# Kernel optimization log

Hardware: AMD Instinct MI355X
Metric: run time of the kernel (lower is better)

The kernel has to match this reference:

```python
import jax, jax.numpy as jnp
import numpy as np

B, C, H, W, D = 2, 96, 64, 64, 32
NUM_HEADS = 8

def setup_inputs() -> dict:
    key = jax.random.key(0)
    kx, kq, kk, kv, kp = jax.random.split(key, 5)
    x = jax.random.normal(kx, (B, C, H, W, D), dtype=jnp.float32)
    # torch nn.Linear weights: [out_features, in_features]; 1x1x1 conv proj as [C_out, C_in]
    s = 0.02
    Wq = jax.random.normal(kq, (C, C), dtype=jnp.float32) * s
    Wk = jax.random.normal(kk, (C, C), dtype=jnp.float32) * s
    Wv = jax.random.normal(kv, (C, C), dtype=jnp.float32) * s
    Wproj = jax.random.normal(kp, (C, C), dtype=jnp.float32) * s
    return {"x": x, "Wq": Wq, "Wk": Wk, "Wv": Wv, "Wproj": Wproj}

def reference(x, Wq, Wk, Wv, Wproj):
    b, c, h, w, d = x.shape
    n = h * w * d
    nh = NUM_HEADS
    hd = c // nh  # head dim (qk_dim == v_dim == dim here)
    # [B, C, H, W, D] -> [B, N, C]
    xf = jnp.transpose(x.reshape(b, c, n), (0, 2, 1))
    def to_heads(W):
        y = jnp.einsum('bnc,oc->bno', xf, W)  # nn.Linear: x @ W^T
        return jnp.transpose(y.reshape(b, n, nh, hd), (0, 2, 1, 3))  # [B, H, N, hd]
    q = to_heads(Wq)
    k = to_heads(Wk)
    v = to_heads(Wv)
    q = jax.nn.softmax(q, axis=-1)   # over head dim
    k = jax.nn.softmax(k, axis=-2)   # over tokens N
    # linear attention: contract over N first -> tiny [B, H, hd, hd] context
    context = jnp.einsum('bhnd,bhne->bhde', k, v)
    attn = jnp.einsum('bhnd,bhde->bhne', q, context)  # [B, H, N, hd]
    out = jnp.transpose(attn, (0, 2, 1, 3)).reshape(b, n, c)  # [B, N, C]
    out = jnp.transpose(out, (0, 2, 1)).reshape(b, c, h, w, d)
    # 1x1x1 conv projection (bias=False) == channel mixing
    out = jnp.einsum('oc,bchwd->bohwd', Wproj, out)
    return out
```

## Files before the change

kernel.cpp:

```cpp
#include <hip/hip_runtime.h>


typedef _Float16 half_t;
typedef _Float16 half8 __attribute__((ext_vector_type(8)));
typedef float f32x4 __attribute__((ext_vector_type(4)));

#define MFMA16 __builtin_amdgcn_mfma_f32_16x16x32_f16
#define NSH 17
#define NP 16

__global__ __launch_bounds__(256, 2)
void p1(const float* __restrict__ x, const float* __restrict__ Wk,
        const float* __restrict__ Wv, float* __restrict__ part) {
  __shared__ __align__(16) char smem[73792];
  half_t* xs  = (half_t*)smem;
  half_t* wsm = (half_t*)(smem + 26624);
  half_t* vl  = (half_t*)smem;
  half_t* ke  = (half_t*)(smem + 46592);

  const int tid  = threadIdx.x;
  const int lane = tid & 63, l15 = lane & 15, quad = lane >> 4, wid = tid >> 6;
  const int b  = blockIdx.x >> 10;
  const int n0 = (blockIdx.x & 1023) << 7;

  {
    const int n = tid & 127, cg = tid >> 7;
    const float* xb = x + (((size_t)(b * 96 + cg * 48)) << NSH) + n0 + n;
#pragma unroll
    for (int i = 0; i < 48; ++i)
      xs[n * 104 + cg * 48 + i] = (half_t)xb[(size_t)i << NSH];
  }
#pragma unroll
  for (int i = 0; i < 36; ++i) {
    int id = i * 256 + tid; int o = id / 96, c = id - o * 96;
    wsm[o * 104 + c] = (half_t)Wk[id];
  }
  __syncthreads();

  f32x4 acc[6][2];
#pragma unroll
  for (int rt = 0; rt < 6; ++rt)
#pragma unroll
    for (int ct = 0; ct < 2; ++ct) acc[rt][ct] = (f32x4){0.f, 0.f, 0.f, 0.f};
#pragma unroll
  for (int ks = 0; ks < 3; ++ks) {
    half8 af[6], bf[2];
#pragma unroll
    for (int rt = 0; rt < 6; ++rt)
      af[rt] = *(const half8*)&wsm[(rt * 16 + l15) * 104 + ks * 32 + quad * 8];
#pragma unroll
    for (int ct = 0; ct < 2; ++ct)
      bf[ct] = *(const half8*)&xs[((wid * 2 + ct) * 16 + l15) * 104 + ks * 32 + quad * 8];
#pragma unroll
    for (int rt = 0; rt < 6; ++rt)
#pragma unroll
      for (int ct = 0; ct < 2; ++ct)
        acc[rt][ct] = MFMA16(af[rt], bf[ct], acc[rt][ct], 0, 0, 0);
  }
#pragma unroll
  for (int rt = 0; rt < 6; ++rt)
#pragma unroll
    for (int ct = 0; ct < 2; ++ct)
#pragma unroll
      for (int i = 0; i < 4; ++i) {
        int row = rt * 16 + quad * 4 + i;
        int col = (wid * 2 + ct) * 16 + l15;
        ke[row * 136 + col] = (half_t)__expf(acc[rt][ct][i]);
      }
  __syncthreads();

#pragma unroll
  for (int i = 0; i < 36; ++i) {
    int id = i * 256 + tid; int o = id / 96, c = id - o * 96;
    wsm[o * 104 + c] = (half_t)Wv[id];
  }
  __syncthreads();

#pragma unroll
  for (int rt = 0; rt < 6; ++rt)
#pragma unroll
    for (int ct = 0; ct < 2; ++ct) acc[rt][ct] = (f32x4){0.f, 0.f, 0.f, 0.f};
#pragma unroll
  for (int ks = 0; ks < 3; ++ks) {
    half8 af[6], bf[2];
#pragma unroll
    for (int rt = 0; rt < 6; ++rt)
      af[rt] = *(const half8*)&wsm[(rt * 16 + l15) * 104 + ks * 32 + quad * 8];
#pragma unroll
    for (int ct = 0; ct < 2; ++ct)
      bf[ct] = *(const half8*)&xs[((wid * 2 + ct) * 16 + l15) * 104 + ks * 32 + quad * 8];
#pragma unroll
    for (int rt = 0; rt < 6; ++rt)
#pragma unroll
      for (int ct = 0; ct < 2; ++ct)
        acc[rt][ct] = MFMA16(af[rt], bf[ct], acc[rt][ct], 0, 0, 0);
  }
  __syncthreads();
#pragma unroll
  for (int rt = 0; rt < 6; ++rt)
#pragma unroll
    for (int ct = 0; ct < 2; ++ct)
#pragma unroll
      for (int i = 0; i < 4; ++i) {
        int row = rt * 16 + quad * 4 + i;
        int col = (wid * 2 + ct) * 16 + l15;
        vl[row * 136 + col] = (half_t)acc[rt][ct][i];
      }
  __syncthreads();

  float* dst = part + (size_t)((blockIdx.x & (NP - 1)) * 2 + b) * 1248;
#pragma unroll
  for (int hh = 0; hh < 2; ++hh) {
    const int h = wid * 2 + hh;
    f32x4 c = (f32x4){0.f, 0.f, 0.f, 0.f};
#pragma unroll
    for (int ks = 0; ks < 4; ++ks) {
      half8 a  = *(const half8*)&ke[(h * 12 + l15) * 136 + ks * 32 + quad * 8];
      half8 bv = *(const half8*)&vl[(h * 12 + l15) * 136 + ks * 32 + quad * 8];
      c = MFMA16(a, bv, c, 0, 0, 0);
    }
#pragma unroll
    for (int i = 0; i < 4; ++i) {
      int d = quad * 4 + i, e = l15;
      if (d < 12 && e < 12) atomicAdd(&dst[h * 144 + d * 12 + e], c[i]);
    }
  }
  if (tid < 96) {
    float s = 0.f;
#pragma unroll
    for (int j = 0; j < 16; ++j) {
      half8 v = *(const half8*)&ke[tid * 136 + j * 8];
#pragma unroll
      for (int e = 0; e < 8; ++e) s += (float)v[e];
    }
    atomicAdd(&dst[1152 + tid], s);
  }
}

__global__ void kB(const float* __restrict__ part, const float* __restrict__ Wproj,
                   float* __restrict__ Mt) {
  const int g = blockIdx.x * 256 + threadIdx.x;
  const int b = g / (96 * 96);
  const int rem = g % (96 * 96);
  const int o = rem / 96;
  const int r = rem % 96;
  const int h = r / 12, d = r % 12;
  float s = 0.f;
#pragma unroll
  for (int p = 0; p < NP; ++p) s += part[(size_t)(p * 2 + b) * 1248 + 1152 + r];
  float acc = 0.f;
#pragma unroll
  for (int e = 0; e < 12; ++e) {
    float ce = 0.f;
#pragma unroll
    for (int p = 0; p < NP; ++p)
      ce += part[(size_t)(p * 2 + b) * 1248 + h * 144 + d * 12 + e];
    acc = fmaf(ce, Wproj[o * 96 + h * 12 + e], acc);
  }
  Mt[(size_t)(b * 96 + o) * 96 + r] = acc / s;
}

__global__ __launch_bounds__(256, 2)
void p3(const float* __restrict__ x, const float* __restrict__ Wq,
        const float* __restrict__ Mt, float* __restrict__ out) {
  __shared__ __align__(16) char smem[66560];
  half_t* xs  = (half_t*)smem;
  half_t* wsm = (half_t*)(smem + 26624);
  half_t* Ms  = (half_t*)(smem + 46592);
  half_t* qs  = (half_t*)smem;

  const int tid  = threadIdx.x;
  const int lane = tid & 63, l15 = lane & 15, quad = lane >> 4, wid = tid >> 6;
  const int b  = blockIdx.x >> 10;
  const int n0 = (blockIdx.x & 1023) << 7;

  {
    const int n = tid & 127, cg = tid >> 7;
    const float* xb = x + (((size_t)(b * 96 + cg * 48)) << NSH) + n0 + n;
#pragma unroll
    for (int i = 0; i < 48; ++i)
      xs[n * 104 + cg * 48 + i] = (half_t)xb[(size_t)i << NSH];
  }
#pragma unroll
  for (int i = 0; i < 36; ++i) {
    int id = i * 256 + tid; int o = id / 96, c = id - o * 96;
    wsm[o * 104 + c] = (half_t)Wq[id];
  }
  {
    const float* mtb = Mt + (size_t)b * 9216;
#pragma unroll
    for (int i = 0; i < 36; ++i) {
      int id = i * 256 + tid; int o = id / 96, r = id - o * 96;
      Ms[o * 104 + r] = (half_t)mtb[id];
    }
  }
  __syncthreads();

  f32x4 acc[6][2];
#pragma unroll
  for (int rt = 0; rt < 6; ++rt)
#pragma unroll
    for (int ct = 0; ct < 2; ++ct) acc[rt][ct] = (f32x4){0.f, 0.f, 0.f, 0.f};
#pragma unroll
  for (int ks = 0; ks < 3; ++ks) {
    half8 af[6], bf[2];
#pragma unroll
    for (int rt = 0; rt < 6; ++rt)
      af[rt] = *(const half8*)&wsm[(rt * 16 + l15) * 104 + ks * 32 + quad * 8];
#pragma unroll
    for (int ct = 0; ct < 2; ++ct)
      bf[ct] = *(const half8*)&xs[((wid * 2 + ct) * 16 + l15) * 104 + ks * 32 + quad * 8];
#pragma unroll
    for (int rt = 0; rt < 6; ++rt)
#pragma unroll
      for (int ct = 0; ct < 2; ++ct)
        acc[rt][ct] = MFMA16(af[rt], bf[ct], acc[rt][ct], 0, 0, 0);
  }
  __syncthreads();
#pragma unroll
  for (int rt = 0; rt < 6; ++rt)
#pragma unroll
    for (int ct = 0; ct < 2; ++ct)
#pragma unroll
      for (int i = 0; i < 4; ++i) {
        int row = rt * 16 + quad * 4 + i;
        int col = (wid * 2 + ct) * 16 + l15;
        qs[col * 104 + row] = (half_t)acc[rt][ct][i];
      }
  __syncthreads();

  {
    const int n = tid & 127, hg = tid >> 7;
    half8 v[6];
#pragma unroll
    for (int j = 0; j < 6; ++j)
      v[j] = *(const half8*)&qs[n * 104 + hg * 48 + j * 8];
    float q[48];
#pragma unroll
    for (int j = 0; j < 6; ++j)
#pragma unroll
      for (int e = 0; e < 8; ++e) q[j * 8 + e] = (float)v[j][e];
#pragma unroll
    for (int hh = 0; hh < 4; ++hh) {
      float* ql = q + hh * 12;
      float m = ql[0];
#pragma unroll
      for (int j = 1; j < 12; ++j) m = fmaxf(m, ql[j]);
      float s = 0.f;
#pragma unroll
      for (int j = 0; j < 12; ++j) { ql[j] = __expf(ql[j] - m); s += ql[j]; }
      const float inv = 1.0f / s;
#pragma unroll
      for (int j = 0; j < 12; ++j) ql[j] *= inv;
    }
#pragma unroll
    for (int j = 0; j < 6; ++j) {
      half8 w;
#pragma unroll
      for (int e = 0; e < 8; ++e) w[e] = (half_t)q[j * 8 + e];
      *(half8*)&qs[n * 104 + hg * 48 + j * 8] = w;
    }
  }
  __syncthreads();

#pragma unroll
  for (int rt = 0; rt < 6; ++rt)
#pragma unroll
    for (int ct = 0; ct < 2; ++ct) acc[rt][ct] = (f32x4){0.f, 0.f, 0.f, 0.f};
#pragma unroll
  for (int ks = 0; ks < 3; ++ks) {
    half8 af[6], bf[2];
#pragma unroll
    for (int rt = 0; rt < 6; ++rt)
      af[rt] = *(const half8*)&Ms[(rt * 16 + l15) * 104 + ks * 32 + quad * 8];
#pragma unroll
    for (int ct = 0; ct < 2; ++ct)
      bf[ct] = *(const half8*)&qs[((wid * 2 + ct) * 16 + l15) * 104 + ks * 32 + quad * 8];
#pragma unroll
    for (int rt = 0; rt < 6; ++rt)
#pragma unroll
      for (int ct = 0; ct < 2; ++ct)
        acc[rt][ct] = MFMA16(af[rt], bf[ct], acc[rt][ct], 0, 0, 0);
  }
#pragma unroll
  for (int rt = 0; rt < 6; ++rt)
#pragma unroll
    for (int ct = 0; ct < 2; ++ct)
#pragma unroll
      for (int i = 0; i < 4; ++i) {
        int row = rt * 16 + quad * 4 + i;
        int col = (wid * 2 + ct) * 16 + l15;
        out[(((size_t)(b * 96 + row)) << NSH) + n0 + col] = acc[rt][ct][i];
      }
}

extern "C" void kernel_launch(void* const* d_in, const int* in_sizes, int n_in,
                              void* d_out, int out_size, void* d_ws, size_t ws_size,
                              hipStream_t stream) {
  const float* x     = (const float*)d_in[0];
  const float* Wq    = (const float*)d_in[1];
  const float* Wk    = (const float*)d_in[2];
  const float* Wv    = (const float*)d_in[3];
  const float* Wproj = (const float*)d_in[4];
  float* out = (float*)d_out;
  float* ws  = (float*)d_ws;

  float* part = ws;
  float* Mt   = ws + NP * 2 * 1248;

  hipMemsetAsync(part, 0, NP * 2 * 1248 * sizeof(float), stream);
  p1<<<2048, 256, 0, stream>>>(x, Wk, Wv, part);
  kB<<<72, 256, 0, stream>>>(part, Wproj, Mt);
  p3<<<2048, 256, 0, stream>>>(x, Wq, Mt, out);
}
```

Measured before the change: 262.2 us.

## Load x straight into MFMA fragments, pre-convert weights to fp16, swizzle LDS

Each lane now loads its x values directly from global memory into MFMA B-fragments in registers, so the x and weight staging through shared memory is gone. The weights are converted to fp16 once by a small kernel and read from global/L2 as A-fragments. The context matrix is stored as fp16. The remaining LDS buffers use an XOR swizzle instead of padding, which cuts LDS use so launch bounds can rise to 3 and 4 blocks per CU. The cost is an extra kernel launch, redundant global weight loads per wave, and higher register pressure from holding 48 x values per lane.

```diff
diff --git a/kernel.cpp b/kernel.cpp
--- a/kernel.cpp
+++ b/kernel.cpp
@@ -9,33 +9,48 @@
 #define NSH 17
 #define NP 16
 
-__global__ __launch_bounds__(256, 2)
-void p1(const float* __restrict__ x, const float* __restrict__ Wk,
-        const float* __restrict__ Wv, float* __restrict__ part) {
-  __shared__ __align__(16) char smem[73792];
-  half_t* xs  = (half_t*)smem;
-  half_t* wsm = (half_t*)(smem + 26624);
-  half_t* vl  = (half_t*)smem;
-  half_t* ke  = (half_t*)(smem + 46592);
+__device__ __forceinline__ int swz(int row, int colh) {
+  return (row * 256 + colh * 2) ^ ((row & 7) << 4);
+}
+
+__global__ void wcvt(const float* __restrict__ Wq, const float* __restrict__ Wk,
+                     const float* __restrict__ Wv, half_t* __restrict__ WqH,
+                     half_t* __restrict__ WkH, half_t* __restrict__ WvH) {
+  const int g = blockIdx.x * 256 + threadIdx.x;
+  WqH[g] = (half_t)Wq[g];
+  WkH[g] = (half_t)Wk[g];
+  WvH[g] = (half_t)Wv[g];
+}
+
+__global__ __launch_bounds__(256, 3)
+void p1(const float* __restrict__ x, const half_t* __restrict__ Wk,
+        const half_t* __restrict__ Wv, float* __restrict__ part) {
+  __shared__ __align__(16) char smem[49152];
 
   const int tid  = threadIdx.x;
   const int lane = tid & 63, l15 = lane & 15, quad = lane >> 4, wid = tid >> 6;
   const int b  = blockIdx.x >> 10;
   const int n0 = (blockIdx.x & 1023) << 7;
 
+  float xv[48];
   {
-    const int n = tid & 127, cg = tid >> 7;
-    const float* xb = x + (((size_t)(b * 96 + cg * 48)) << NSH) + n0 + n;
-#pragma unroll
-    for (int i = 0; i < 48; ++i)
-      xs[n * 104 + cg * 48 + i] = (half_t)xb[(size_t)i << NSH];
-  }
-#pragma unroll
-  for (int i = 0; i < 36; ++i) {
-    int id = i * 256 + tid; int o = id / 96, c = id - o * 96;
-    wsm[o * 104 + c] = (half_t)Wk[id];
-  }
-  __syncthreads();
+    const float* xb = x + (((size_t)(b * 96 + quad * 8)) << NSH) + n0 + wid * 32 + l15;
+#pragma unroll
+    for (int ks = 0; ks < 3; ++ks)
+#pragma unroll
+      for (int j = 0; j < 8; ++j)
+#pragma unroll
+        for (int ct = 0; ct < 2; ++ct)
+          xv[(ks * 8 + j) * 2 + ct] = xb[(((size_t)(ks * 32 + j)) << NSH) + ct * 16];
+  }
+  half8 bf[3][2];
+#pragma unroll
+  for (int ks = 0; ks < 3; ++ks)
+#pragma unroll
+    for (int ct = 0; ct < 2; ++ct)
+#pragma unroll
+      for (int j = 0; j < 8; ++j)
+        bf[ks][ct][j] = (half_t)xv[(ks * 8 + j) * 2 + ct];
 
   f32x4 acc[6][2];
 #pragma unroll
@@ -44,18 +59,15 @@
     for (int ct = 0; ct < 2; ++ct) acc[rt][ct] = (f32x4){0.f, 0.f, 0.f, 0.f};
 #pragma unroll
   for (int ks = 0; ks < 3; ++ks) {
-    half8 af[6], bf[2];
-#pragma unroll
-    for (int rt = 0; rt < 6; ++rt)
-      af[rt] = *(const half8*)&wsm[(rt * 16 + l15) * 104 + ks * 32 + quad * 8];
-#pragma unroll
-    for (int ct = 0; ct < 2; ++ct)
-      bf[ct] = *(const half8*)&xs[((wid * 2 + ct) * 16 + l15) * 104 + ks * 32 + quad * 8];
+    half8 af[6];
+#pragma unroll
+    for (int rt = 0; rt < 6; ++rt)
+      af[rt] = *(const half8*)&Wk[(rt * 16 + l15) * 96 + ks * 32 + quad * 8];
 #pragma unroll
     for (int rt = 0; rt < 6; ++rt)
 #pragma unroll
       for (int ct = 0; ct < 2; ++ct)
-        acc[rt][ct] = MFMA16(af[rt], bf[ct], acc[rt][ct], 0, 0, 0);
+        acc[rt][ct] = MFMA16(af[rt], bf[ks][ct], acc[rt][ct], 0, 0, 0);
   }
 #pragma unroll
   for (int rt = 0; rt < 6; ++rt)
@@ -65,16 +77,8 @@
       for (int i = 0; i < 4; ++i) {
         int row = rt * 16 + quad * 4 + i;
         int col = (wid * 2 + ct) * 16 + l15;
-        ke[row * 136 + col] = (half_t)__expf(acc[rt][ct][i]);
+        *(half_t*)(smem + swz(row, col)) = (half_t)__expf(acc[rt][ct][i]);
       }
-  __syncthreads();
-
-#pragma unroll
-  for (int i = 0; i < 36; ++i) {
-    int id = i * 256 + tid; int o = id / 96, c = id - o * 96;
-    wsm[o * 104 + c] = (half_t)Wv[id];
-  }
-  __syncthreads();
 
 #pragma unroll
   for (int rt = 0; rt < 6; ++rt)
@@ -82,20 +86,16 @@
     for (int ct = 0; ct < 2; ++ct) acc[rt][ct] = (f32x4){0.f, 0.f, 0.f, 0.f};
 #pragma unroll
   for (int ks = 0; ks < 3; ++ks) {
-    half8 af[6], bf[2];
-#pragma unroll
-    for (int rt = 0; rt < 6; ++rt)
-      af[rt] = *(const half8*)&wsm[(rt * 16 + l15) * 104 + ks * 32 + quad * 8];
-#pragma unroll
-    for (int ct = 0; ct < 2; ++ct)
-      bf[ct] = *(const half8*)&xs[((wid * 2 + ct) * 16 + l15) * 104 + ks * 32 + quad * 8];
+    half8 af[6];
+#pragma unroll
+    for (int rt = 0; rt < 6; ++rt)
+      af[rt] = *(const half8*)&Wv[(rt * 16 + l15) * 96 + ks * 32 + quad * 8];
 #pragma unroll
     for (int rt = 0; rt < 6; ++rt)
 #pragma unroll
       for (int ct = 0; ct < 2; ++ct)
-        acc[rt][ct] = MFMA16(af[rt], bf[ct], acc[rt][ct], 0, 0, 0);
-  }
-  __syncthreads();
+        acc[rt][ct] = MFMA16(af[rt], bf[ks][ct], acc[rt][ct], 0, 0, 0);
+  }
 #pragma unroll
   for (int rt = 0; rt < 6; ++rt)
 #pragma unroll
@@ -104,7 +104,7 @@
       for (int i = 0; i < 4; ++i) {
         int row = rt * 16 + quad * 4 + i;
         int col = (wid * 2 + ct) * 16 + l15;
-        vl[row * 136 + col] = (half_t)acc[rt][ct][i];
+        *(half_t*)(smem + 24576 + swz(row, col)) = (half_t)acc[rt][ct][i];
       }
   __syncthreads();
 
@@ -112,11 +112,13 @@
 #pragma unroll
   for (int hh = 0; hh < 2; ++hh) {
     const int h = wid * 2 + hh;
+    int row = h * 12 + l15; row = row > 95 ? 95 : row;
     f32x4 c = (f32x4){0.f, 0.f, 0.f, 0.f};
 #pragma unroll
     for (int ks = 0; ks < 4; ++ks) {
-      half8 a  = *(const half8*)&ke[(h * 12 + l15) * 136 + ks * 32 + quad * 8];
-      half8 bv = *(const half8*)&vl[(h * 12 + l15) * 136 + ks * 32 + quad * 8];
+      const int off = swz(row, ks * 32 + quad * 8);
+      half8 a  = *(const half8*)(smem + off);
+      half8 bv = *(const half8*)(smem + 24576 + off);
       c = MFMA16(a, bv, c, 0, 0, 0);
     }
 #pragma unroll
@@ -129,7 +131,7 @@
     float s = 0.f;
 #pragma unroll
     for (int j = 0; j < 16; ++j) {
-      half8 v = *(const half8*)&ke[tid * 136 + j * 8];
+      half8 v = *(const half8*)(smem + swz(tid, j * 8));
 #pragma unroll
       for (int e = 0; e < 8; ++e) s += (float)v[e];
     }
@@ -138,7 +140,7 @@
 }
 
 __global__ void kB(const float* __restrict__ part, const float* __restrict__ Wproj,
-                   float* __restrict__ Mt) {
+                   half_t* __restrict__ Mt) {
   const int g = blockIdx.x * 256 + threadIdx.x;
   const int b = g / (96 * 96);
   const int rem = g % (96 * 96);
@@ -157,44 +159,38 @@
       ce += part[(size_t)(p * 2 + b) * 1248 + h * 144 + d * 12 + e];
     acc = fmaf(ce, Wproj[o * 96 + h * 12 + e], acc);
   }
-  Mt[(size_t)(b * 96 + o) * 96 + r] = acc / s;
-}
-
-__global__ __launch_bounds__(256, 2)
-void p3(const float* __restrict__ x, const float* __restrict__ Wq,
-        const float* __restrict__ Mt, float* __restrict__ out) {
-  __shared__ __align__(16) char smem[66560];
-  half_t* xs  = (half_t*)smem;
-  half_t* wsm = (half_t*)(smem + 26624);
-  half_t* Ms  = (half_t*)(smem + 46592);
-  half_t* qs  = (half_t*)smem;
+  Mt[(size_t)(b * 96 + o) * 96 + r] = (half_t)(acc / s);
+}
+
+__global__ __launch_bounds__(256, 4)
+void p3(const float* __restrict__ x, const half_t* __restrict__ Wq,
+        const half_t* __restrict__ Mt, float* __restrict__ out) {
+  __shared__ __align__(16) char smem[32768];
 
   const int tid  = threadIdx.x;
   const int lane = tid & 63, l15 = lane & 15, quad = lane >> 4, wid = tid >> 6;
   const int b  = blockIdx.x >> 10;
   const int n0 = (blockIdx.x & 1023) << 7;
 
+  float xv[48];
   {
-    const int n = tid & 127, cg = tid >> 7;
-    const float* xb = x + (((size_t)(b * 96 + cg * 48)) << NSH) + n0 + n;
-#pragma unroll
-    for (int i = 0; i < 48; ++i)
-      xs[n * 104 + cg * 48 + i] = (half_t)xb[(size_t)i << NSH];
-  }
-#pragma unroll
-  for (int i = 0; i < 36; ++i) {
-    int id = i * 256 + tid; int o = id / 96, c = id - o * 96;
-    wsm[o * 104 + c] = (half_t)Wq[id];
-  }
-  {
-    const float* mtb = Mt + (size_t)b * 9216;
-#pragma unroll
-    for (int i = 0; i < 36; ++i) {
-      int id = i * 256 + tid; int o = id / 96, r = id - o * 96;
-      Ms[o * 104 + r] = (half_t)mtb[id];
-    }
-  }
-  __syncthreads();
+    const float* xb = x + (((size_t)(b * 96 + quad * 8)) << NSH) + n0 + wid * 32 + l15;
+#pragma unroll
+    for (int ks = 0; ks < 3; ++ks)
+#pragma unroll
+      for (int j = 0; j < 8; ++j)
+#pragma unroll
+        for (int ct = 0; ct < 2; ++ct)
+          xv[(ks * 8 + j) * 2 + ct] = xb[(((size_t)(ks * 32 + j)) << NSH) + ct * 16];
+  }
+  half8 bf[3][2];
+#pragma unroll
+  for (int ks = 0; ks < 3; ++ks)
+#pragma unroll
+    for (int ct = 0; ct < 2; ++ct)
+#pragma unroll
+      for (int j = 0; j < 8; ++j)
+        bf[ks][ct][j] = (half_t)xv[(ks * 8 + j) * 2 + ct];
 
   f32x4 acc[6][2];
 #pragma unroll
@@ -203,20 +199,16 @@
     for (int ct = 0; ct < 2; ++ct) acc[rt][ct] = (f32x4){0.f, 0.f, 0.f, 0.f};
 #pragma unroll
   for (int ks = 0; ks < 3; ++ks) {
-    half8 af[6], bf[2];
-#pragma unroll
-    for (int rt = 0; rt < 6; ++rt)
-      af[rt] = *(const half8*)&wsm[(rt * 16 + l15) * 104 + ks * 32 + quad * 8];
-#pragma unroll
-    for (int ct = 0; ct < 2; ++ct)
-      bf[ct] = *(const half8*)&xs[((wid * 2 + ct) * 16 + l15) * 104 + ks * 32 + quad * 8];
+    half8 af[6];
+#pragma unroll
+    for (int rt = 0; rt < 6; ++rt)
+      af[rt] = *(const half8*)&Wq[(rt * 16 + l15) * 96 + ks * 32 + quad * 8];
 #pragma unroll
     for (int rt = 0; rt < 6; ++rt)
 #pragma unroll
       for (int ct = 0; ct < 2; ++ct)
-        acc[rt][ct] = MFMA16(af[rt], bf[ct], acc[rt][ct], 0, 0, 0);
-  }
-  __syncthreads();
+        acc[rt][ct] = MFMA16(af[rt], bf[ks][ct], acc[rt][ct], 0, 0, 0);
+  }
 #pragma unroll
   for (int rt = 0; rt < 6; ++rt)
 #pragma unroll
@@ -225,21 +217,19 @@
       for (int i = 0; i < 4; ++i) {
         int row = rt * 16 + quad * 4 + i;
         int col = (wid * 2 + ct) * 16 + l15;
-        qs[col * 104 + row] = (half_t)acc[rt][ct][i];
+        *(half_t*)(smem + swz(col, row)) = (half_t)acc[rt][ct][i];
       }
   __syncthreads();
 
   {
     const int n = tid & 127, hg = tid >> 7;
-    half8 v[6];
-#pragma unroll
-    for (int j = 0; j < 6; ++j)
-      v[j] = *(const half8*)&qs[n * 104 + hg * 48 + j * 8];
     float q[48];
 #pragma unroll
-    for (int j = 0; j < 6; ++j)
-#pragma unroll
-      for (int e = 0; e < 8; ++e) q[j * 8 + e] = (float)v[j][e];
+    for (int j = 0; j < 6; ++j) {
+      half8 v = *(const half8*)(smem + swz(n, hg * 48 + j * 8));
+#pragma unroll
+      for (int e = 0; e < 8; ++e) q[j * 8 + e] = (float)v[e];
+    }
 #pragma unroll
     for (int hh = 0; hh < 4; ++hh) {
       float* ql = q + hh * 12;
@@ -258,7 +248,7 @@
       half8 w;
 #pragma unroll
       for (int e = 0; e < 8; ++e) w[e] = (half_t)q[j * 8 + e];
-      *(half8*)&qs[n * 104 + hg * 48 + j * 8] = w;
+      *(half8*)(smem + swz(n, hg * 48 + j * 8)) = w;
     }
   }
   __syncthreads();
@@ -269,18 +259,18 @@
     for (int ct = 0; ct < 2; ++ct) acc[rt][ct] = (f32x4){0.f, 0.f, 0.f, 0.f};
 #pragma unroll
   for (int ks = 0; ks < 3; ++ks) {
-    half8 af[6], bf[2];
-#pragma unroll
-    for (int rt = 0; rt < 6; ++rt)
-      af[rt] = *(const half8*)&Ms[(rt * 16 + l15) * 104 + ks * 32 + quad * 8];
-#pragma unroll
-    for (int ct = 0; ct < 2; ++ct)
-      bf[ct] = *(const half8*)&qs[((wid * 2 + ct) * 16 + l15) * 104 + ks * 32 + quad * 8];
+    half8 af[6], bq[2];
+#pragma unroll
+    for (int rt = 0; rt < 6; ++rt)
+      af[rt] = *(const half8*)&Mt[(size_t)b * 9216 + (rt * 16 + l15) * 96 + ks * 32 + quad * 8];
+#pragma unroll
+    for (int ct = 0; ct < 2; ++ct)
+      bq[ct] = *(const half8*)(smem + swz((wid * 2 + ct) * 16 + l15, ks * 32 + quad * 8));
 #pragma unroll
     for (int rt = 0; rt < 6; ++rt)
 #pragma unroll
       for (int ct = 0; ct < 2; ++ct)
-        acc[rt][ct] = MFMA16(af[rt], bf[ct], acc[rt][ct], 0, 0, 0);
+        acc[rt][ct] = MFMA16(af[rt], bq[ct], acc[rt][ct], 0, 0, 0);
   }
 #pragma unroll
   for (int rt = 0; rt < 6; ++rt)
@@ -305,11 +295,15 @@
   float* out = (float*)d_out;
   float* ws  = (float*)d_ws;
 
-  float* part = ws;
-  float* Mt   = ws + NP * 2 * 1248;
+  float*  part = ws;
+  half_t* Mt   = (half_t*)(ws + NP * 2 * 1248);
+  half_t* WqH  = (half_t*)(ws + NP * 2 * 1248 + 9216);
+  half_t* WkH  = WqH + 9216;
+  half_t* WvH  = WkH + 9216;
 
   hipMemsetAsync(part, 0, NP * 2 * 1248 * sizeof(float), stream);
-  p1<<<2048, 256, 0, stream>>>(x, Wk, Wv, part);
+  wcvt<<<36, 256, 0, stream>>>(Wq, Wk, Wv, WqH, WkH, WvH);
+  p1<<<2048, 256, 0, stream>>>(x, WkH, WvH, part);
   kB<<<72, 256, 0, stream>>>(part, Wproj, Mt);
-  p3<<<2048, 256, 0, stream>>>(x, Wq, Mt, out);
-}
+  p3<<<2048, 256, 0, stream>>>(x, WqH, Mt, out);
+}
```

New measurement: 246.3 us. -6.0%, faster.
